# Optimization experiments

Hardware: AMD Instinct MI355X
Metric: run time of the kernel (lower is better)

Reference implementation:

```python
import jax, jax.numpy as jnp
import numpy as np

EPS = 1e-5
B, S, D = 4, 2048, 128
BALL_SCALE = 0.05  # keeps points inside the unit Poincare ball for c=1


def setup_inputs() -> dict:
    key = jax.random.key(0)
    kq, kk, kv = jax.random.split(key, 3)
    q = jax.random.normal(kq, (B, S, D), dtype=jnp.float32) * BALL_SCALE
    k = jax.random.normal(kk, (B, S, D), dtype=jnp.float32) * BALL_SCALE
    v_tangent = jax.random.normal(kv, (B, S, D), dtype=jnp.float32)
    c = jnp.asarray(1.0, dtype=jnp.float32)
    beta = jnp.asarray(0.0, dtype=jnp.float32)            # nn.Parameter init 0.0
    attention_bias = jnp.asarray(0.0, dtype=jnp.float32)  # nn.Parameter init 0.0
    return {"q": q, "k": k, "v_tangent": v_tangent, "c": c,
            "beta": beta, "attention_bias": attention_bias}


def reference(q, k, v_tangent, c, beta, attention_bias):
    sqrt_c = jnp.sqrt(c)

    # --- pairwise Poincare distance (all fp32, as in the torch autocast block) ---
    x_norm_sq = jnp.sum(q * q, axis=-1, keepdims=True)            # (B,S,1)
    y_norm_sq = jnp.sum(k * k, axis=-1, keepdims=True)            # (B,S,1)
    xy_dot = jnp.einsum('bsd,btd->bst', q, k)                     # (B,S,S)
    y_norm_sq_t = jnp.swapaxes(y_norm_sq, -2, -1)                 # (B,1,S)
    diff_norm_sq = x_norm_sq - 2.0 * xy_dot + y_norm_sq_t         # ||x-y||^2, (B,S,S)
    denom = (1.0 - c * x_norm_sq) * (1.0 - c * y_norm_sq_t)       # (B,S,S)
    arg = 1.0 + 2.0 * c * diff_norm_sq / jnp.maximum(denom, EPS)
    dist = jnp.arccosh(jnp.maximum(arg, 1.0 + EPS)) / sqrt_c      # (B,S,S)

    # --- attention ---
    beta_positive = jax.nn.softplus(beta)
    attention_scores = -beta_positive * dist - attention_bias
    attention_weights = jax.nn.softmax(attention_scores, axis=-1)  # (B,S,S)
    output_tangent = jnp.einsum('bst,btd->bsd', attention_weights, v_tangent)

    # --- exp map at origin ---
    v_norm = jnp.maximum(
        jnp.sqrt(jnp.sum(output_tangent * output_tangent, axis=-1, keepdims=True)), EPS)
    output_hyperbolic = (jnp.tanh(sqrt_c * v_norm) / sqrt_c) * (output_tangent / v_norm)

    return output_hyperbolic, attention_weights
```

## Files before the change

kernel.cpp:

```cpp
#include <hip/hip_runtime.h>
#include <math.h>

#define B_ 4
#define S_ 2048
#define D_ 128
#define EPSF 1e-5f
#define BN 128
#define PSB 272

typedef __attribute__((ext_vector_type(8))) short short8;
typedef __attribute__((ext_vector_type(4))) float f32x4;

static __device__ __forceinline__ unsigned short f2bf(float f) {
    unsigned u = __float_as_uint(f);
    return (unsigned short)((u + 0x7fffu + ((u >> 16) & 1u)) >> 16);
}


__global__ __launch_bounds__(256) void convqk_kernel(const float* __restrict__ q,
                                                     const float* __restrict__ k,
                                                     float* __restrict__ qn, float* __restrict__ kn,
                                                     unsigned* __restrict__ Qb, unsigned* __restrict__ Kb) {
    int row = blockIdx.x * 4 + (threadIdx.x >> 6);
    int lane = threadIdx.x & 63;
    const int NR = B_ * S_;
    bool isQ = row < NR;
    int r = isQ ? row : row - NR;
    float2 v = ((const float2*)(isQ ? q : k))[(size_t)r * 64 + lane];
    unsigned pk = (unsigned)f2bf(v.x) | ((unsigned)f2bf(v.y) << 16);
    float nrm = v.x * v.x + v.y * v.y;
#pragma unroll
    for (int m = 1; m <= 32; m <<= 1) nrm += __shfl_xor(nrm, m, 64);
    if (isQ) {
        Qb[(size_t)r * 64 + lane] = pk;
        if (lane == 0) qn[r] = nrm;
    } else {
        int c = lane >> 2;
        int cs = c ^ (r & 7);
        Kb[(size_t)r * 64 + cs * 4 + (lane & 3)] = pk;
        if (lane == 0) kn[r] = nrm;
    }
}

__global__ __launch_bounds__(256) void convv_kernel(const float* __restrict__ v, uint4* __restrict__ Vtb) {
    __shared__ unsigned short Vs[128 * 132];
    int b = blockIdx.x >> 4;
    int t = blockIdx.x & 15;
    int tid = threadIdx.x;
    const float* src = v + ((size_t)b * S_ + t * 128) * D_;
    int d4 = tid & 31, key0 = tid >> 5;
#pragma unroll
    for (int it = 0; it < 16; ++it) {
        int key = key0 + it * 8;
        float4 f = *(const float4*)(src + (size_t)key * D_ + d4 * 4);
        unsigned short* dst = &Vs[key * 132 + d4 * 4];
        dst[0] = f2bf(f.x); dst[1] = f2bf(f.y); dst[2] = f2bf(f.z); dst[3] = f2bf(f.w);
    }
    __syncthreads();
    uint4* tile = Vtb + (size_t)blockIdx.x * (128 * 16);
    int d = tid & 127;
    int cl = tid >> 7;
#pragma unroll
    for (int it = 0; it < 8; ++it) {
        int c = cl + it * 2;
        int kb = c * 8;
        unsigned short e0 = Vs[(kb + 0) * 132 + d], e1 = Vs[(kb + 1) * 132 + d];
        unsigned short e2 = Vs[(kb + 2) * 132 + d], e3 = Vs[(kb + 3) * 132 + d];
        unsigned short e4 = Vs[(kb + 4) * 132 + d], e5 = Vs[(kb + 5) * 132 + d];
        unsigned short e6 = Vs[(kb + 6) * 132 + d], e7 = Vs[(kb + 7) * 132 + d];
        uint4 o;
        o.x = (unsigned)e0 | ((unsigned)e1 << 16);
        o.y = (unsigned)e2 | ((unsigned)e3 << 16);
        o.z = (unsigned)e4 | ((unsigned)e5 << 16);
        o.w = (unsigned)e6 | ((unsigned)e7 << 16);
        tile[d * 16 + (c ^ (d & 7))] = o;
    }
}


__global__ __launch_bounds__(512, 2) void hattn_kernel(
    const unsigned short* __restrict__ Qb, const char* __restrict__ Kb, const char* __restrict__ Vtb,
    const float* __restrict__ qn, const float* __restrict__ kn,
    const float* __restrict__ cp, const float* __restrict__ betap, const float* __restrict__ biasp,
    float* __restrict__ lws, float* __restrict__ houtg, float* __restrict__ woutg) {

    __shared__ __align__(1024) char smem[75136];
    char* KsB = smem;
    char* VtB = smem + 32768;
    char* PsB = smem + 65536;
    float* kn_s  = (float*)(smem + 74240);
    float* qn_s  = (float*)(smem + 74752);
    float* l_row = (float*)(smem + 74880);
    float* nsq_s = (float*)(smem + 75008);

    const int tid = threadIdx.x;
    const int lane = tid & 63, wave = tid >> 6;
    const int wm = wave & 1, wn = wave >> 1;
    const int lm = lane & 15, quad = lane >> 4;

    int xcd = blockIdx.x & 7;
    int b = xcd >> 1;
    int rb = (blockIdx.x >> 3) * 2 + (xcd & 1);
    int s0 = rb * 32;
    const size_t bS = (size_t)b * S_;

    const float cc = cp[0], beta = betap[0], bias = biasp[0];
    const float beta_pos = fmaxf(beta, 0.f) + log1pf(__expf(-fabsf(beta)));
    const float sqrt_c = sqrtf(cc);
    const float inv_sqrt_c = 1.f / sqrt_c;

    if (tid < 32) {
        qn_s[tid] = qn[bS + s0 + tid];
        l_row[tid] = 0.f;
        nsq_s[tid] = 0.f;
    }

    short8 aq[4];
    {
        const unsigned short* qrow = Qb + (bS + s0 + wm * 16 + lm) * D_;
#pragma unroll
        for (int ks = 0; ks < 4; ++ks)
            aq[ks] = *(const short8*)(qrow + ks * 32 + quad * 8);
    }

    f32x4 o0 = {0.f, 0.f, 0.f, 0.f}, o1 = {0.f, 0.f, 0.f, 0.f};

    const char* KbBase = Kb + bS * 256;
    const char* VtBase = Vtb + (size_t)b * 16 * 32768;

    for (int t = 0; t < S_ / BN; ++t) {
        int t0 = t * BN;
        __syncthreads();
        {
            const uint4* ksrc = (const uint4*)(KbBase + (size_t)t0 * 256);
            const uint4* vsrc = (const uint4*)(VtBase + (size_t)t * 32768);
            uint4* kd = (uint4*)KsB;
            uint4* vd = (uint4*)VtB;
#pragma unroll
            for (int i = 0; i < 4; ++i) {
                kd[tid + i * 512] = ksrc[tid + i * 512];
                vd[tid + i * 512] = vsrc[tid + i * 512];
            }
            if (tid < BN) kn_s[tid] = kn[bS + t0 + tid];
        }
        __syncthreads();

        f32x4 acc0 = {0.f, 0.f, 0.f, 0.f}, acc1 = {0.f, 0.f, 0.f, 0.f};
#pragma unroll
        for (int ks = 0; ks < 4; ++ks) {
            int n0 = wn * 32 + lm;
            int c = ks * 4 + quad;
            short8 b0 = *(const short8*)(KsB + n0 * 256 + ((c ^ (n0 & 7)) * 16));
            int n1 = n0 + 16;
            short8 b1 = *(const short8*)(KsB + n1 * 256 + ((c ^ (n1 & 7)) * 16));
            acc0 = __builtin_amdgcn_mfma_f32_16x16x32_bf16(aq[ks], b0, acc0, 0, 0, 0);
            acc1 = __builtin_amdgcn_mfma_f32_16x16x32_bf16(aq[ks], b1, acc1, 0, 0, 0);
        }

        float lp[4];
#pragma unroll
        for (int r = 0; r < 4; ++r) {
            int row = wm * 16 + quad * 4 + r;
            float xn = qn_s[row];
            float fx = 1.f - cc * xn;
            float p0, p1;
#pragma unroll
            for (int nt = 0; nt < 2; ++nt) {
                int col = wn * 32 + nt * 16 + lm;
                float dot = (nt == 0) ? acc0[r] : acc1[r];
                float yn = kn_s[col];
                float diff = xn - 2.f * dot + yn;
                float den = fmaxf(fx * (1.f - cc * yn), EPSF);
                float arg = fmaf(2.f * cc * diff, __builtin_amdgcn_rcpf(den), 1.f);
                arg = fmaxf(arg, 1.f + EPSF);
                float dist = __logf(arg + sqrtf(arg * arg - 1.f)) * inv_sqrt_c;
                float p = __expf(fmaf(-beta_pos, dist, -bias));
                woutg[(bS + s0 + row) * S_ + t0 + col] = p;
                *(unsigned short*)(PsB + row * PSB + col * 2) = f2bf(p);
                if (nt == 0) p0 = p; else p1 = p;
            }
            lp[r] = p0 + p1;
        }
#pragma unroll
        for (int r = 0; r < 4; ++r) {
            float s = lp[r];
#pragma unroll
            for (int m = 1; m <= 8; m <<= 1) s += __shfl_xor(s, m, 64);
            if (lm == 0) atomicAdd(&l_row[wm * 16 + quad * 4 + r], s);
        }
        __syncthreads();

#pragma unroll
        for (int ks = 0; ks < 4; ++ks) {
            short8 ap = *(const short8*)(PsB + (wm * 16 + lm) * PSB + (ks * 32 + quad * 8) * 2);
            int d0 = wn * 32 + lm;
            int c = ks * 4 + quad;
            short8 v0 = *(const short8*)(VtB + d0 * 256 + ((c ^ (d0 & 7)) * 16));
            int d1 = d0 + 16;
            short8 v1 = *(const short8*)(VtB + d1 * 256 + ((c ^ (d1 & 7)) * 16));
            o0 = __builtin_amdgcn_mfma_f32_16x16x32_bf16(ap, v0, o0, 0, 0, 0);
            o1 = __builtin_amdgcn_mfma_f32_16x16x32_bf16(ap, v1, o1, 0, 0, 0);
        }
    }
    __syncthreads();

    float xs0[4], xs1[4];
#pragma unroll
    for (int r = 0; r < 4; ++r) {
        int row = wm * 16 + quad * 4 + r;
        float linv = __builtin_amdgcn_rcpf(l_row[row]);
        float x0 = o0[r] * linv, x1 = o1[r] * linv;
        xs0[r] = x0; xs1[r] = x1;
        float np = x0 * x0 + x1 * x1;
#pragma unroll
        for (int m = 1; m <= 8; m <<= 1) np += __shfl_xor(np, m, 64);
        if (lm == 0) atomicAdd(&nsq_s[row], np);
    }
    if (tid < 32) lws[bS + s0 + tid] = l_row[tid];
    __syncthreads();
#pragma unroll
    for (int r = 0; r < 4; ++r) {
        int row = wm * 16 + quad * 4 + r;
        float vn = fmaxf(sqrtf(nsq_s[row]), EPSF);
        float a = sqrt_c * vn;
        float th = 1.f - 2.f * __builtin_amdgcn_rcpf(__expf(2.f * a) + 1.f);
        float sc = th / a;
        houtg[(bS + s0 + row) * D_ + wn * 32 + lm] = xs0[r] * sc;
        houtg[(bS + s0 + row) * D_ + wn * 32 + 16 + lm] = xs1[r] * sc;
    }
}

__global__ __launch_bounds__(256) void wnorm_kernel(float* __restrict__ w,
                                                    const float* __restrict__ lws) {
    size_t idx = (size_t)blockIdx.x * 256 + threadIdx.x;
    int row = (int)(idx >> 9);
    float linv = 1.f / lws[row];
    float4* p = (float4*)w + idx;
    float4 v = *p;
    v.x *= linv; v.y *= linv; v.z *= linv; v.w *= linv;
    *p = v;
}


__global__ __launch_bounds__(256) void norms_kernel(const float* __restrict__ q,
                                                    const float* __restrict__ k,
                                                    float* __restrict__ ws) {
    int row = blockIdx.x * 4 + (threadIdx.x >> 6);
    int lane = threadIdx.x & 63;
    const int NR = B_ * S_;
    const float* src = (row < NR) ? q : k;
    int r = (row < NR) ? row : row - NR;
    const float* p = src + (size_t)r * D_;
    float x0 = p[lane], x1 = p[lane + 64];
    float a = x0 * x0 + x1 * x1;
#pragma unroll
    for (int m = 1; m <= 32; m <<= 1) a += __shfl_xor(a, m, 64);
    if (lane == 0) ws[row] = a;
}

__global__ __launch_bounds__(256) void attn_kernel(
    const float* __restrict__ qg, const float* __restrict__ kg, const float* __restrict__ vg,
    const float* __restrict__ cp, const float* __restrict__ betap, const float* __restrict__ biasp,
    const float* __restrict__ ws, float* __restrict__ lws,
    float* __restrict__ houtg, float* __restrict__ woutg) {

    __shared__ float Qs[32][D_ + 4];
    __shared__ float KsT[D_][64 + 4];
    __shared__ float Vs[64][D_];
    __shared__ float Ps[32][64 + 4];
    __shared__ float qn_s[32];
    __shared__ float kn_s[64];
    __shared__ float l_row[32];

    const int tid = threadIdx.x;
    int xcd = blockIdx.x & 7;
    int b = xcd >> 1;
    int rb = (blockIdx.x >> 3) * 2 + (xcd & 1);
    int s0 = rb * 32;

    const float cc = cp[0];
    const float beta = betap[0];
    const float bias = biasp[0];
    const float beta_pos = fmaxf(beta, 0.f) + log1pf(__expf(-fabsf(beta)));
    const float sqrt_c = sqrtf(cc);
    const float inv_sqrt_c = 1.f / sqrt_c;

    const float* qn = ws;
    const float* kn = ws + B_ * S_;
    const size_t bS = (size_t)b * S_;

    {
        int d4 = tid & 31, rr0 = tid >> 5;
#pragma unroll
        for (int it = 0; it < 4; ++it) {
            int rr = it * 8 + rr0;
            float4 v = *(const float4*)(qg + (bS + s0 + rr) * D_ + d4 * 4);
            *(float4*)&Qs[rr][d4 * 4] = v;
        }
    }
    if (tid < 32) { qn_s[tid] = qn[bS + s0 + tid]; l_row[tid] = 0.f; }

    const int cg = tid & 15, rg = tid >> 4;
    const int c0 = cg * 4, r0 = rg * 2;
    const int cgv = tid & 31, rgv = tid >> 5;
    const int c0v = cgv * 4, r0v = rgv * 4;

    float o[4][4];
#pragma unroll
    for (int i = 0; i < 4; ++i)
#pragma unroll
        for (int j = 0; j < 4; ++j) o[i][j] = 0.f;

    for (int t0 = 0; t0 < S_; t0 += 64) {
        __syncthreads();
        {
            int d = tid & 127, seg = tid >> 7;
#pragma unroll
            for (int it = 0; it < 8; ++it) {
                int cbase = it * 8 + seg * 4;
                float f0 = kg[(bS + t0 + cbase + 0) * D_ + d];
                float f1 = kg[(bS + t0 + cbase + 1) * D_ + d];
                float f2 = kg[(bS + t0 + cbase + 2) * D_ + d];
                float f3 = kg[(bS + t0 + cbase + 3) * D_ + d];
                float4 w = {f0, f1, f2, f3};
                *(float4*)&KsT[d][cbase] = w;
            }
        }
        {
            int d4 = tid & 31, rv = tid >> 5;
#pragma unroll
            for (int it = 0; it < 8; ++it) {
                int rr = it * 8 + rv;
                *(float4*)&Vs[rr][d4 * 4] = *(const float4*)(vg + (bS + t0 + rr) * D_ + d4 * 4);
            }
        }
        if (tid < 64) kn_s[tid] = kn[bS + t0 + tid];
        __syncthreads();

        float acc[2][4];
#pragma unroll
        for (int i = 0; i < 2; ++i)
#pragma unroll
            for (int j = 0; j < 4; ++j) acc[i][j] = 0.f;

#pragma unroll 4
        for (int d = 0; d < D_; ++d) {
            float4 kv = *(const float4*)&KsT[d][c0];
            float q0 = Qs[r0][d];
            float q1 = Qs[r0 + 1][d];
            acc[0][0] = fmaf(q0, kv.x, acc[0][0]);
            acc[0][1] = fmaf(q0, kv.y, acc[0][1]);
            acc[0][2] = fmaf(q0, kv.z, acc[0][2]);
            acc[0][3] = fmaf(q0, kv.w, acc[0][3]);
            acc[1][0] = fmaf(q1, kv.x, acc[1][0]);
            acc[1][1] = fmaf(q1, kv.y, acc[1][1]);
            acc[1][2] = fmaf(q1, kv.z, acc[1][2]);
            acc[1][3] = fmaf(q1, kv.w, acc[1][3]);
        }

        float lp[2] = {0.f, 0.f};
#pragma unroll
        for (int i = 0; i < 2; ++i) {
            int r = r0 + i;
            float xn = qn_s[r];
            float one_m_cxn = 1.f - cc * xn;
            float4 pv;
            float* pp = &pv.x;
#pragma unroll
            for (int j = 0; j < 4; ++j) {
                float yn = kn_s[c0 + j];
                float diff = xn - 2.f * acc[i][j] + yn;
                float den = one_m_cxn * (1.f - cc * yn);
                den = fmaxf(den, EPSF);
                float arg = 1.f + 2.f * cc * diff / den;
                arg = fmaxf(arg, 1.f + EPSF);
                float dist = __logf(arg + sqrtf(arg * arg - 1.f)) * inv_sqrt_c;
                float p = __expf(fmaf(-beta_pos, dist, -bias));
                pp[j] = p;
                lp[i] += p;
            }
            *(float4*)&Ps[r][c0] = pv;
            *(float4*)(woutg + (bS + s0 + r) * S_ + t0 + c0) = pv;
        }
#pragma unroll
        for (int m = 1; m <= 8; m <<= 1) {
            lp[0] += __shfl_xor(lp[0], m, 64);
            lp[1] += __shfl_xor(lp[1], m, 64);
        }
        if (cg == 0) { l_row[r0] += lp[0]; l_row[r0 + 1] += lp[1]; }
        __syncthreads();

#pragma unroll 4
        for (int kk = 0; kk < 64; ++kk) {
            float4 vv = *(const float4*)&Vs[kk][c0v];
            float pa0 = Ps[r0v + 0][kk];
            float pa1 = Ps[r0v + 1][kk];
            float pa2 = Ps[r0v + 2][kk];
            float pa3 = Ps[r0v + 3][kk];
            o[0][0] = fmaf(pa0, vv.x, o[0][0]);
            o[0][1] = fmaf(pa0, vv.y, o[0][1]);
            o[0][2] = fmaf(pa0, vv.z, o[0][2]);
            o[0][3] = fmaf(pa0, vv.w, o[0][3]);
            o[1][0] = fmaf(pa1, vv.x, o[1][0]);
            o[1][1] = fmaf(pa1, vv.y, o[1][1]);
            o[1][2] = fmaf(pa1, vv.z, o[1][2]);
            o[1][3] = fmaf(pa1, vv.w, o[1][3]);
            o[2][0] = fmaf(pa2, vv.x, o[2][0]);
            o[2][1] = fmaf(pa2, vv.y, o[2][1]);
            o[2][2] = fmaf(pa2, vv.z, o[2][2]);
            o[2][3] = fmaf(pa2, vv.w, o[2][3]);
            o[3][0] = fmaf(pa3, vv.x, o[3][0]);
            o[3][1] = fmaf(pa3, vv.y, o[3][1]);
            o[3][2] = fmaf(pa3, vv.z, o[3][2]);
            o[3][3] = fmaf(pa3, vv.w, o[3][3]);
        }
    }
    __syncthreads();

#pragma unroll
    for (int i = 0; i < 4; ++i) {
        int r = r0v + i;
        float l = l_row[r];
        float linv = 1.f / l;
        float x0 = o[i][0] * linv;
        float x1 = o[i][1] * linv;
        float x2 = o[i][2] * linv;
        float x3 = o[i][3] * linv;
        float nsq = x0 * x0 + x1 * x1 + x2 * x2 + x3 * x3;
#pragma unroll
        for (int m = 1; m <= 16; m <<= 1) nsq += __shfl_xor(nsq, m, 64);
        float vn = fmaxf(sqrtf(nsq), EPSF);
        float sc = tanhf(sqrt_c * vn) * inv_sqrt_c / vn;
        float4 outv = {x0 * sc, x1 * sc, x2 * sc, x3 * sc};
        *(float4*)(houtg + (bS + s0 + r) * D_ + c0v) = outv;
        if (cgv == 0) lws[bS + s0 + r] = l;
    }
}


extern "C" void kernel_launch(void* const* d_in, const int* in_sizes, int n_in,
                              void* d_out, int out_size, void* d_ws, size_t ws_size,
                              hipStream_t stream) {
    const float* q    = (const float*)d_in[0];
    const float* k    = (const float*)d_in[1];
    const float* v    = (const float*)d_in[2];
    const float* c    = (const float*)d_in[3];
    const float* beta = (const float*)d_in[4];
    const float* ab   = (const float*)d_in[5];

    float* out  = (float*)d_out;
    float* hout = out;
    float* wout = out + (size_t)B_ * S_ * D_;

    float* qn  = (float*)d_ws;
    float* kn  = qn + B_ * S_;
    float* lws = kn + B_ * S_;
    char*  wsb = (char*)d_ws;
    const size_t QB_OFF = 98304;
    const size_t KB_OFF = QB_OFF + 2097152;
    const size_t VT_OFF = KB_OFF + 2097152;
    const size_t NEED   = VT_OFF + 2097152;

    if (ws_size >= NEED) {
        unsigned* Qb = (unsigned*)(wsb + QB_OFF);
        unsigned* Kb = (unsigned*)(wsb + KB_OFF);
        uint4*   Vtb = (uint4*)(wsb + VT_OFF);
        convqk_kernel<<<4096, 256, 0, stream>>>(q, k, qn, kn, Qb, Kb);
        convv_kernel<<<64, 256, 0, stream>>>(v, Vtb);
        hattn_kernel<<<256, 512, 0, stream>>>((const unsigned short*)Qb, (const char*)Kb,
                                              (const char*)Vtb, qn, kn, c, beta, ab,
                                              lws, hout, wout);
        wnorm_kernel<<<(B_ * S_ * S_ / 4) / 256, 256, 0, stream>>>(wout, lws);
    } else {
        norms_kernel<<<(2 * B_ * S_) / 4, 256, 0, stream>>>(q, k, qn);
        attn_kernel<<<(B_ * S_) / 32, 256, 0, stream>>>(q, k, v, c, beta, ab, qn, lws, hout, wout);
        wnorm_kernel<<<(B_ * S_ * S_ / 4) / 256, 256, 0, stream>>>(wout, lws);
    }
}
```

Measured before the change: 166.7 us.

## Split key range across two blocks and stage bf16 probabilities in workspace

Adds a new attention kernel that splits each row block's key range in half across two blocks, writing partial outputs and atomically accumulating row sums. Unnormalized probabilities are staged as bf16 in workspace, and a separate pass expands and normalizes them into the fp32 weight output, so the large fp32 matrix is no longer written twice. K and V tiles load with direct global-to-LDS loads, and the exp/log math uses exp2/log2 intrinsics. The cost is an extra epilogue kernel, partial-output traffic, and a larger workspace requirement, and the path only runs when that workspace is available.

```diff
diff --git a/kernel.cpp b/kernel.cpp
--- a/kernel.cpp
+++ b/kernel.cpp
@@ -16,10 +16,16 @@
     return (unsigned short)((u + 0x7fffu + ((u >> 16) & 1u)) >> 16);
 }
 
+static __device__ __forceinline__ void gload_lds16(const void* g, void* l) {
+    __builtin_amdgcn_global_load_lds((const __attribute__((address_space(1))) unsigned*)g,
+                                     (__attribute__((address_space(3))) unsigned*)l, 16, 0, 0);
+}
+
 
 __global__ __launch_bounds__(256) void convqk_kernel(const float* __restrict__ q,
                                                      const float* __restrict__ k,
                                                      float* __restrict__ qn, float* __restrict__ kn,
+                                                     float* __restrict__ lws,
                                                      unsigned* __restrict__ Qb, unsigned* __restrict__ Kb) {
     int row = blockIdx.x * 4 + (threadIdx.x >> 6);
     int lane = threadIdx.x & 63;
@@ -34,6 +40,7 @@
     if (isQ) {
         Qb[(size_t)r * 64 + lane] = pk;
         if (lane == 0) qn[r] = nrm;
+        if (lane == 1) lws[r] = 0.f;
     } else {
         int c = lane >> 2;
         int cs = c ^ (r & 7);
@@ -75,6 +82,201 @@
         o.w = (unsigned)e6 | ((unsigned)e7 << 16);
         tile[d * 16 + (c ^ (d & 7))] = o;
     }
+}
+
+
+__global__ __launch_bounds__(512, 2) void hattn2_kernel(
+    const unsigned short* __restrict__ Qb, const char* __restrict__ Kb, const char* __restrict__ Vtb,
+    const float* __restrict__ qn, const float* __restrict__ kn,
+    const float* __restrict__ cp, const float* __restrict__ betap, const float* __restrict__ biasp,
+    float* __restrict__ lws, float* __restrict__ Opart, uint4* __restrict__ Pws) {
+
+    __shared__ __align__(1024) char smem[76032];
+    char* KsB = smem;
+    char* VtB = smem + 32768;
+    char* PsB = smem + 65536;
+    float* yn_s  = (float*)(smem + 74240);
+    float* gy_s  = (float*)(smem + 74752);
+    float* xn_s  = (float*)(smem + 75264);
+    float* rx_s  = (float*)(smem + 75392);
+    float* l_row = (float*)(smem + 75520);
+
+    const int tid = threadIdx.x;
+    const int lane = tid & 63, wave = tid >> 6;
+    const int wm = wave & 1, wn = wave >> 1;
+    const int lm = lane & 15, quad = lane >> 4;
+
+    const int th = blockIdx.x & 1;
+    const int b = (blockIdx.x >> 1) & 3;
+    const int rb = blockIdx.x >> 3;
+    const int s0 = rb * 32;
+    const size_t bS = (size_t)b * S_;
+
+    const float cc = cp[0], beta = betap[0], bias = biasp[0];
+    const float beta_pos = fmaxf(beta, 0.f) + log1pf(__expf(-fabsf(beta)));
+    const float sqrt_c = sqrtf(cc);
+    const float bneg = -beta_pos / sqrt_c;
+    const float bias2 = -bias * 1.442695040888963f;
+    const float onepe = 1.f + EPSF;
+    const float c2 = 2.f * cc;
+
+    if (tid < 32) {
+        float xn = qn[bS + s0 + tid];
+        xn_s[tid] = xn;
+        rx_s[tid] = c2 * __builtin_amdgcn_rcpf(1.f - cc * xn);
+        l_row[tid] = 0.f;
+    }
+
+    short8 aq[4];
+    {
+        const unsigned short* qrow = Qb + (bS + s0 + wm * 16 + lm) * D_;
+#pragma unroll
+        for (int ks = 0; ks < 4; ++ks)
+            aq[ks] = *(const short8*)(qrow + ks * 32 + quad * 8);
+    }
+
+    f32x4 o0 = {0.f, 0.f, 0.f, 0.f}, o1 = {0.f, 0.f, 0.f, 0.f};
+
+    const char* KbBase = Kb + bS * 256;
+    const char* VtBase = Vtb + (size_t)b * 16 * 32768;
+
+    for (int it = 0; it < 8; ++it) {
+        int t = th * 8 + it;
+        int t0 = t * BN;
+        __syncthreads();
+        {
+            const char* ks = KbBase + (size_t)t0 * 256;
+            const char* vs = VtBase + (size_t)t * 32768;
+#pragma unroll
+            for (int j = 0; j < 4; ++j) {
+                int off = (tid + j * 512) * 16;
+                gload_lds16(ks + off, KsB + off);
+                gload_lds16(vs + off, VtB + off);
+            }
+            if (tid < BN) {
+                float yn = kn[bS + t0 + tid];
+                yn_s[tid] = yn;
+                gy_s[tid] = __builtin_amdgcn_rcpf(1.f - cc * yn);
+            }
+        }
+        __syncthreads();
+
+        f32x4 acc0 = {0.f, 0.f, 0.f, 0.f}, acc1 = {0.f, 0.f, 0.f, 0.f};
+#pragma unroll
+        for (int ks = 0; ks < 4; ++ks) {
+            int n0 = wn * 32 + lm;
+            int c = ks * 4 + quad;
+            short8 b0 = *(const short8*)(KsB + n0 * 256 + ((c ^ (n0 & 7)) * 16));
+            int n1 = n0 + 16;
+            short8 b1 = *(const short8*)(KsB + n1 * 256 + ((c ^ (n1 & 7)) * 16));
+            acc0 = __builtin_amdgcn_mfma_f32_16x16x32_bf16(aq[ks], b0, acc0, 0, 0, 0);
+            acc1 = __builtin_amdgcn_mfma_f32_16x16x32_bf16(aq[ks], b1, acc1, 0, 0, 0);
+        }
+
+        int col0 = wn * 32 + lm, col1 = col0 + 16;
+        float yn0 = yn_s[col0], gy0 = gy_s[col0];
+        float yn1 = yn_s[col1], gy1 = gy_s[col1];
+#pragma unroll
+        for (int r = 0; r < 4; ++r) {
+            int row = wm * 16 + quad * 4 + r;
+            float xn = xn_s[row];
+            float rx = rx_s[row];
+
+            float diff0 = fmaf(-2.f, acc0[r], xn + yn0);
+            float arg0 = fmaf(diff0 * gy0, rx, 1.f);
+            arg0 = fmaxf(arg0, onepe);
+            float w0 = arg0 + sqrtf(fmaf(arg0, arg0, -1.f));
+            float p0 = __builtin_amdgcn_exp2f(fmaf(bneg, __builtin_amdgcn_logf(w0), bias2));
+
+            float diff1 = fmaf(-2.f, acc1[r], xn + yn1);
+            float arg1 = fmaf(diff1 * gy1, rx, 1.f);
+            arg1 = fmaxf(arg1, onepe);
+            float w1 = arg1 + sqrtf(fmaf(arg1, arg1, -1.f));
+            float p1 = __builtin_amdgcn_exp2f(fmaf(bneg, __builtin_amdgcn_logf(w1), bias2));
+
+            *(unsigned short*)(PsB + row * PSB + col0 * 2) = f2bf(p0);
+            *(unsigned short*)(PsB + row * PSB + col1 * 2) = f2bf(p1);
+
+            float s = p0 + p1;
+#pragma unroll
+            for (int m = 1; m <= 8; m <<= 1) s += __shfl_xor(s, m, 64);
+            if (lm == 0) atomicAdd(&l_row[row], s);
+        }
+        __syncthreads();
+
+        {
+            int row = tid >> 4, chunk = tid & 15;
+            uint4 pv = *(const uint4*)(PsB + row * PSB + chunk * 16);
+            Pws[(((bS + s0 + row) * S_ + t0) >> 3) + chunk] = pv;
+        }
+
+#pragma unroll
+        for (int ks = 0; ks < 4; ++ks) {
+            short8 ap = *(const short8*)(PsB + (wm * 16 + lm) * PSB + (ks * 32 + quad * 8) * 2);
+            int d0 = wn * 32 + lm;
+            int c = ks * 4 + quad;
+            short8 v0 = *(const short8*)(VtB + d0 * 256 + ((c ^ (d0 & 7)) * 16));
+            int d1 = d0 + 16;
+            short8 v1 = *(const short8*)(VtB + d1 * 256 + ((c ^ (d1 & 7)) * 16));
+            o0 = __builtin_amdgcn_mfma_f32_16x16x32_bf16(ap, v0, o0, 0, 0, 0);
+            o1 = __builtin_amdgcn_mfma_f32_16x16x32_bf16(ap, v1, o1, 0, 0, 0);
+        }
+    }
+    __syncthreads();
+
+    float* op = Opart + (size_t)th * (B_ * S_ * D_) + (bS + s0) * D_;
+#pragma unroll
+    for (int r = 0; r < 4; ++r) {
+        int row = wm * 16 + quad * 4 + r;
+        op[(size_t)row * D_ + wn * 32 + lm] = o0[r];
+        op[(size_t)row * D_ + wn * 32 + 16 + lm] = o1[r];
+    }
+    if (tid < 32) atomicAdd(&lws[bS + s0 + tid], l_row[tid]);
+}
+
+__global__ __launch_bounds__(256) void hepi_kernel(const float* __restrict__ Opart,
+                                                   const float* __restrict__ lws,
+                                                   const float* __restrict__ cp,
+                                                   float* __restrict__ hout) {
+    int row = blockIdx.x * 4 + (threadIdx.x >> 6);
+    int lane = threadIdx.x & 63;
+    const float cc = cp[0];
+    const float sqrt_c = sqrtf(cc);
+    float2 a = ((const float2*)(Opart + (size_t)row * D_))[lane];
+    float2 b = ((const float2*)(Opart + (size_t)(B_ * S_ * D_) + (size_t)row * D_))[lane];
+    float linv = 1.f / lws[row];
+    float x0 = (a.x + b.x) * linv;
+    float x1 = (a.y + b.y) * linv;
+    float np = x0 * x0 + x1 * x1;
+#pragma unroll
+    for (int m = 1; m <= 32; m <<= 1) np += __shfl_xor(np, m, 64);
+    float vn = fmaxf(sqrtf(np), EPSF);
+    float aa = sqrt_c * vn;
+    float t = 1.f - 2.f / (__expf(2.f * aa) + 1.f);
+    float sc = t / aa;
+    float2 o = {x0 * sc, x1 * sc};
+    ((float2*)(hout + (size_t)row * D_))[lane] = o;
+}
+
+__global__ __launch_bounds__(256) void wnorm2_kernel(const uint4* __restrict__ Pws,
+                                                     const float* __restrict__ lws,
+                                                     float* __restrict__ w) {
+    size_t idx = (size_t)blockIdx.x * 256 + threadIdx.x;
+    int row = (int)(idx >> 8);
+    float linv = 1.f / lws[row];
+    uint4 u = Pws[idx];
+    float4 f0, f1;
+    f0.x = __uint_as_float(u.x << 16) * linv;
+    f0.y = __uint_as_float(u.x & 0xffff0000u) * linv;
+    f0.z = __uint_as_float(u.y << 16) * linv;
+    f0.w = __uint_as_float(u.y & 0xffff0000u) * linv;
+    f1.x = __uint_as_float(u.z << 16) * linv;
+    f1.y = __uint_as_float(u.z & 0xffff0000u) * linv;
+    f1.z = __uint_as_float(u.w << 16) * linv;
+    f1.w = __uint_as_float(u.w & 0xffff0000u) * linv;
+    float4* out = (float4*)w + idx * 2;
+    out[0] = f0;
+    out[1] = f1;
 }
 
 
@@ -242,202 +444,6 @@
 }
 
 
-__global__ __launch_bounds__(256) void norms_kernel(const float* __restrict__ q,
-                                                    const float* __restrict__ k,
-                                                    float* __restrict__ ws) {
-    int row = blockIdx.x * 4 + (threadIdx.x >> 6);
-    int lane = threadIdx.x & 63;
-    const int NR = B_ * S_;
-    const float* src = (row < NR) ? q : k;
-    int r = (row < NR) ? row : row - NR;
-    const float* p = src + (size_t)r * D_;
-    float x0 = p[lane], x1 = p[lane + 64];
-    float a = x0 * x0 + x1 * x1;
-#pragma unroll
-    for (int m = 1; m <= 32; m <<= 1) a += __shfl_xor(a, m, 64);
-    if (lane == 0) ws[row] = a;
-}
-
-__global__ __launch_bounds__(256) void attn_kernel(
-    const float* __restrict__ qg, const float* __restrict__ kg, const float* __restrict__ vg,
-    const float* __restrict__ cp, const float* __restrict__ betap, const float* __restrict__ biasp,
-    const float* __restrict__ ws, float* __restrict__ lws,
-    float* __restrict__ houtg, float* __restrict__ woutg) {
-
-    __shared__ float Qs[32][D_ + 4];
-    __shared__ float KsT[D_][64 + 4];
-    __shared__ float Vs[64][D_];
-    __shared__ float Ps[32][64 + 4];
-    __shared__ float qn_s[32];
-    __shared__ float kn_s[64];
-    __shared__ float l_row[32];
-
-    const int tid = threadIdx.x;
-    int xcd = blockIdx.x & 7;
-    int b = xcd >> 1;
-    int rb = (blockIdx.x >> 3) * 2 + (xcd & 1);
-    int s0 = rb * 32;
-
-    const float cc = cp[0];
-    const float beta = betap[0];
-    const float bias = biasp[0];
-    const float beta_pos = fmaxf(beta, 0.f) + log1pf(__expf(-fabsf(beta)));
-    const float sqrt_c = sqrtf(cc);
-    const float inv_sqrt_c = 1.f / sqrt_c;
-
-    const float* qn = ws;
-    const float* kn = ws + B_ * S_;
-    const size_t bS = (size_t)b * S_;
-
-    {
-        int d4 = tid & 31, rr0 = tid >> 5;
-#pragma unroll
-        for (int it = 0; it < 4; ++it) {
-            int rr = it * 8 + rr0;
-            float4 v = *(const float4*)(qg + (bS + s0 + rr) * D_ + d4 * 4);
-            *(float4*)&Qs[rr][d4 * 4] = v;
-        }
-    }
-    if (tid < 32) { qn_s[tid] = qn[bS + s0 + tid]; l_row[tid] = 0.f; }
-
-    const int cg = tid & 15, rg = tid >> 4;
-    const int c0 = cg * 4, r0 = rg * 2;
-    const int cgv = tid & 31, rgv = tid >> 5;
-    const int c0v = cgv * 4, r0v = rgv * 4;
-
-    float o[4][4];
-#pragma unroll
-    for (int i = 0; i < 4; ++i)
-#pragma unroll
-        for (int j = 0; j < 4; ++j) o[i][j] = 0.f;
-
-    for (int t0 = 0; t0 < S_; t0 += 64) {
-        __syncthreads();
-        {
-            int d = tid & 127, seg = tid >> 7;
-#pragma unroll
-            for (int it = 0; it < 8; ++it) {
-                int cbase = it * 8 + seg * 4;
-                float f0 = kg[(bS + t0 + cbase + 0) * D_ + d];
-                float f1 = kg[(bS + t0 + cbase + 1) * D_ + d];
-                float f2 = kg[(bS + t0 + cbase + 2) * D_ + d];
-                float f3 = kg[(bS + t0 + cbase + 3) * D_ + d];
-                float4 w = {f0, f1, f2, f3};
-                *(float4*)&KsT[d][cbase] = w;
-            }
-        }
-        {
-            int d4 = tid & 31, rv = tid >> 5;
-#pragma unroll
-            for (int it = 0; it < 8; ++it) {
-                int rr = it * 8 + rv;
-                *(float4*)&Vs[rr][d4 * 4] = *(const float4*)(vg + (bS + t0 + rr) * D_ + d4 * 4);
-            }
-        }
-        if (tid < 64) kn_s[tid] = kn[bS + t0 + tid];
-        __syncthreads();
-
-        float acc[2][4];
-#pragma unroll
-        for (int i = 0; i < 2; ++i)
-#pragma unroll
-            for (int j = 0; j < 4; ++j) acc[i][j] = 0.f;
-
-#pragma unroll 4
-        for (int d = 0; d < D_; ++d) {
-            float4 kv = *(const float4*)&KsT[d][c0];
-            float q0 = Qs[r0][d];
-            float q1 = Qs[r0 + 1][d];
-            acc[0][0] = fmaf(q0, kv.x, acc[0][0]);
-            acc[0][1] = fmaf(q0, kv.y, acc[0][1]);
-            acc[0][2] = fmaf(q0, kv.z, acc[0][2]);
-            acc[0][3] = fmaf(q0, kv.w, acc[0][3]);
-            acc[1][0] = fmaf(q1, kv.x, acc[1][0]);
-            acc[1][1] = fmaf(q1, kv.y, acc[1][1]);
-            acc[1][2] = fmaf(q1, kv.z, acc[1][2]);
-            acc[1][3] = fmaf(q1, kv.w, acc[1][3]);
-        }
-
-        float lp[2] = {0.f, 0.f};
-#pragma unroll
-        for (int i = 0; i < 2; ++i) {
-            int r = r0 + i;
-            float xn = qn_s[r];
-            float one_m_cxn = 1.f - cc * xn;
-            float4 pv;
-            float* pp = &pv.x;
-#pragma unroll
-            for (int j = 0; j < 4; ++j) {
-                float yn = kn_s[c0 + j];
-                float diff = xn - 2.f * acc[i][j] + yn;
-                float den = one_m_cxn * (1.f - cc * yn);
-                den = fmaxf(den, EPSF);
-                float arg = 1.f + 2.f * cc * diff / den;
-                arg = fmaxf(arg, 1.f + EPSF);
-                float dist = __logf(arg + sqrtf(arg * arg - 1.f)) * inv_sqrt_c;
-                float p = __expf(fmaf(-beta_pos, dist, -bias));
-                pp[j] = p;
-                lp[i] += p;
-            }
-            *(float4*)&Ps[r][c0] = pv;
-            *(float4*)(woutg + (bS + s0 + r) * S_ + t0 + c0) = pv;
-        }
-#pragma unroll
-        for (int m = 1; m <= 8; m <<= 1) {
-            lp[0] += __shfl_xor(lp[0], m, 64);
-            lp[1] += __shfl_xor(lp[1], m, 64);
-        }
-        if (cg == 0) { l_row[r0] += lp[0]; l_row[r0 + 1] += lp[1]; }
-        __syncthreads();
-
-#pragma unroll 4
-        for (int kk = 0; kk < 64; ++kk) {
-            float4 vv = *(const float4*)&Vs[kk][c0v];
-            float pa0 = Ps[r0v + 0][kk];
-            float pa1 = Ps[r0v + 1][kk];
-            float pa2 = Ps[r0v + 2][kk];
-            float pa3 = Ps[r0v + 3][kk];
-            o[0][0] = fmaf(pa0, vv.x, o[0][0]);
-            o[0][1] = fmaf(pa0, vv.y, o[0][1]);
-            o[0][2] = fmaf(pa0, vv.z, o[0][2]);
-            o[0][3] = fmaf(pa0, vv.w, o[0][3]);
-            o[1][0] = fmaf(pa1, vv.x, o[1][0]);
-            o[1][1] = fmaf(pa1, vv.y, o[1][1]);
-            o[1][2] = fmaf(pa1, vv.z, o[1][2]);
-            o[1][3] = fmaf(pa1, vv.w, o[1][3]);
-            o[2][0] = fmaf(pa2, vv.x, o[2][0]);
-            o[2][1] = fmaf(pa2, vv.y, o[2][1]);
-            o[2][2] = fmaf(pa2, vv.z, o[2][2]);
-            o[2][3] = fmaf(pa2, vv.w, o[2][3]);
-            o[3][0] = fmaf(pa3, vv.x, o[3][0]);
-            o[3][1] = fmaf(pa3, vv.y, o[3][1]);
-            o[3][2] = fmaf(pa3, vv.z, o[3][2]);
-            o[3][3] = fmaf(pa3, vv.w, o[3][3]);
-        }
-    }
-    __syncthreads();
-
-#pragma unroll
-    for (int i = 0; i < 4; ++i) {
-        int r = r0v + i;
-        float l = l_row[r];
-        float linv = 1.f / l;
-        float x0 = o[i][0] * linv;
-        float x1 = o[i][1] * linv;
-        float x2 = o[i][2] * linv;
-        float x3 = o[i][3] * linv;
-        float nsq = x0 * x0 + x1 * x1 + x2 * x2 + x3 * x3;
-#pragma unroll
-        for (int m = 1; m <= 16; m <<= 1) nsq += __shfl_xor(nsq, m, 64);
-        float vn = fmaxf(sqrtf(nsq), EPSF);
-        float sc = tanhf(sqrt_c * vn) * inv_sqrt_c / vn;
-        float4 outv = {x0 * sc, x1 * sc, x2 * sc, x3 * sc};
-        *(float4*)(houtg + (bS + s0 + r) * D_ + c0v) = outv;
-        if (cgv == 0) lws[bS + s0 + r] = l;
-    }
-}
-
-
 extern "C" void kernel_launch(void* const* d_in, const int* in_sizes, int n_in,
                               void* d_out, int out_size, void* d_ws, size_t ws_size,
                               hipStream_t stream) {
@@ -459,21 +465,31 @@
     const size_t QB_OFF = 98304;
     const size_t KB_OFF = QB_OFF + 2097152;
     const size_t VT_OFF = KB_OFF + 2097152;
-    const size_t NEED   = VT_OFF + 2097152;
-
-    if (ws_size >= NEED) {
-        unsigned* Qb = (unsigned*)(wsb + QB_OFF);
-        unsigned* Kb = (unsigned*)(wsb + KB_OFF);
-        uint4*   Vtb = (uint4*)(wsb + VT_OFF);
-        convqk_kernel<<<4096, 256, 0, stream>>>(q, k, qn, kn, Qb, Kb);
+    const size_t NEED1  = VT_OFF + 2097152;
+    const size_t OP_OFF = NEED1;
+    const size_t PW_OFF = OP_OFF + 2u * B_ * S_ * D_ * 4;
+    const size_t NEED2  = PW_OFF + (size_t)B_ * S_ * S_ * 2;
+
+    unsigned* Qb = (unsigned*)(wsb + QB_OFF);
+    unsigned* Kb = (unsigned*)(wsb + KB_OFF);
+    uint4*   Vtb = (uint4*)(wsb + VT_OFF);
+
+    if (ws_size >= NEED2) {
+        float* Opart = (float*)(wsb + OP_OFF);
+        uint4* Pws   = (uint4*)(wsb + PW_OFF);
+        convqk_kernel<<<4096, 256, 0, stream>>>(q, k, qn, kn, lws, Qb, Kb);
+        convv_kernel<<<64, 256, 0, stream>>>(v, Vtb);
+        hattn2_kernel<<<512, 512, 0, stream>>>((const unsigned short*)Qb, (const char*)Kb,
+                                               (const char*)Vtb, qn, kn, c, beta, ab,
+                                               lws, Opart, Pws);
+        hepi_kernel<<<2048, 256, 0, stream>>>(Opart, lws, c, hout);
+        wnorm2_kernel<<<8192, 256, 0, stream>>>(Pws, lws, wout);
+    } else {
+        convqk_kernel<<<4096, 256, 0, stream>>>(q, k, qn, kn, lws, Qb, Kb);
         convv_kernel<<<64, 256, 0, stream>>>(v, Vtb);
         hattn_kernel<<<256, 512, 0, stream>>>((const unsigned short*)Qb, (const char*)Kb,
                                               (const char*)Vtb, qn, kn, c, beta, ab,
                                               lws, hout, wout);
         wnorm_kernel<<<(B_ * S_ * S_ / 4) / 256, 256, 0, stream>>>(wout, lws);
-    } else {
-        norms_kernel<<<(2 * B_ * S_) / 4, 256, 0, stream>>>(q, k, qn);
-        attn_kernel<<<(B_ * S_) / 32, 256, 0, stream>>>(q, k, v, c, beta, ab, qn, lws, hout, wout);
-        wnorm_kernel<<<(B_ * S_ * S_ / 4) / 256, 256, 0, stream>>>(wout, lws);
-    }
-}
+    }
+}
```

Result: faster. 147.5 us (-11.5%).
